# Optimization experiments

Measured on AMD Instinct MI355X. Metric: run time of the kernel, lower is better.

## Reference

```python
import jax, jax.numpy as jnp
import numpy as np

D_MODEL = 1024
N_HEADS = 16
D_K = D_MODEL // N_HEADS


def setup_inputs() -> dict:
    key = jax.random.key(0)
    ks = jax.random.split(key, 9)
    B, S, D = 2, 2048, D_MODEL
    q = jax.random.normal(ks[0], (B, S, D), dtype=jnp.float32)
    v = jax.random.normal(ks[1], (B, S, D), dtype=jnp.float32)
    k = jax.random.normal(ks[2], (B, S, D), dtype=jnp.float32)
    att_mask = jnp.zeros((B, S, S), dtype=jnp.float32)
    seq_mask = jax.random.uniform(ks[3], (B, S, S), dtype=jnp.float32)
    scale = 1.0 / np.sqrt(D)
    Wq = jax.random.normal(ks[4], (D, D), dtype=jnp.float32) * scale
    Wk = jax.random.normal(ks[5], (D, D), dtype=jnp.float32) * scale
    Wv = jax.random.normal(ks[6], (D, D), dtype=jnp.float32) * scale
    Wo = jax.random.normal(ks[7], (D, D), dtype=jnp.float32) * scale
    return {"q": q, "v": v, "k": k, "att_mask": att_mask, "seq_mask": seq_mask,
            "Wq": Wq, "Wk": Wk, "Wv": Wv, "Wo": Wo}


def _split_heads(x, B):
    # [B, S, D] -> [B, H, S, d_k]
    return x.reshape(B, -1, N_HEADS, D_K).transpose(0, 2, 1, 3)


def reference(q, v, k, att_mask, seq_mask, Wq, Wk, Wv, Wo):
    B = q.shape[0]
    qh = _split_heads(q @ Wq, B)
    kh = _split_heads(k @ Wk, B)
    vh = _split_heads(v @ Wv, B)
    # scores: [B, H, Sq, Sk]
    scores = jnp.einsum('bhqd,bhkd->bhqk', qh, kh) / jnp.sqrt(jnp.float32(D_K))
    scores = scores + att_mask[:, None]
    attn = jax.nn.softmax(scores, axis=-1)
    attn = attn * seq_mask[:, None]  # post-softmax multiplicative mask
    out = jnp.einsum('bhqk,bhkd->bhqd', attn, vh)
    out = out.transpose(0, 2, 1, 3).reshape(B, -1, D_MODEL)
    return out @ Wo
```

## Files before the change

### kernel.cpp

```cpp
#include <hip/hip_runtime.h>
#include <cstddef>

typedef __attribute__((ext_vector_type(8))) short s16x8;
typedef __attribute__((ext_vector_type(4))) float f32x4;
typedef __attribute__((ext_vector_type(4))) unsigned short us4;

static __device__ __forceinline__ float bf2f(unsigned short u) {
    union { unsigned u; float f; } v;
    v.u = ((unsigned)u) << 16;
    return v.f;
}

static __device__ __forceinline__ unsigned short f2bf(float f) {
    union { float f; unsigned u; } v;
    v.f = f;
    unsigned r = v.u + 0x7fffu + ((v.u >> 16) & 1u);
    return (unsigned short)(r >> 16);
}

static __device__ __forceinline__ unsigned short f2bf_fast(float f) {
    unsigned r;
    asm("v_cvt_pk_bf16_f32 %0, %1, %2" : "=v"(r) : "v"(f), "v"(f));
    return (unsigned short)r;
}

#if __has_builtin(__builtin_amdgcn_exp2f)
#define EXP2F(x) __builtin_amdgcn_exp2f(x)
#else
#define EXP2F(x) exp2f(x)
#endif

typedef const __attribute__((address_space(1))) unsigned int* as1_cu32p;
typedef __attribute__((address_space(3))) unsigned int* as3_u32p;
static __device__ __forceinline__ void async16(const void* g, void* l) {
    __builtin_amdgcn_global_load_lds((as1_cu32p)g, (as3_u32p)l, 16, 0, 0);
}

static __device__ __forceinline__ float ldf(const unsigned short* p, size_t i) { return bf2f(p[i]); }
static __device__ __forceinline__ float ldf(const float* p, size_t i) { return p[i]; }
static __device__ __forceinline__ void stf(unsigned short* p, size_t i, float v) { p[i] = f2bf(v); }
static __device__ __forceinline__ void stf(float* p, size_t i, float v) { p[i] = v; }

__global__ __launch_bounds__(256) void probe_dtype(
    const unsigned short* __restrict__ q, unsigned* __restrict__ flags)
{
    __shared__ float red[256];
    const int t = threadIdx.x;
    float m = 0.0f;
    for (int i = t; i < 16384; i += 256) {
        float x = fabsf(bf2f(q[i]));
        if (!(x == x)) x = 1.0e30f;
        m = fmaxf(m, x);
    }
    red[t] = m;
    __syncthreads();
    for (int s = 128; s > 0; s >>= 1) {
        if (t < s) red[t] = fmaxf(red[t], red[t + s]);
        __syncthreads();
    }
    if (t == 0) {
        flags[0] = (red[0] < 1000.0f) ? 0u : 1u;
        flags[1] = 0u;
    }
}

__global__ __launch_bounds__(256) void probe_zero(
    const uint4* __restrict__ m, unsigned* __restrict__ flags)
{
    const unsigned dt = flags[0];
    const size_t n = dt ? 2097152u : 1048576u;
    unsigned acc = 0;
    for (size_t i = (size_t)blockIdx.x * 256 + threadIdx.x; i < n;
         i += (size_t)gridDim.x * 256) {
        uint4 v = m[i];
        acc |= v.x | v.y | v.z | v.w;
    }
    if (acc) atomicOr(&flags[1], 1u);
}

__global__ __launch_bounds__(256) void cvt3_f32_bf16(
    const float4* __restrict__ s0, us4* __restrict__ d0,
    const float4* __restrict__ s1, us4* __restrict__ d1,
    const float4* __restrict__ s2, us4* __restrict__ d2,
    unsigned n4, const unsigned* __restrict__ flags)
{
    if (flags[0] != 1u) return;
    const float4* s = (blockIdx.y == 0) ? s0 : (blockIdx.y == 1) ? s1 : s2;
    us4* d = (blockIdx.y == 0) ? d0 : (blockIdx.y == 1) ? d1 : d2;
    for (unsigned i = blockIdx.x * 256u + threadIdx.x; i < n4;
         i += gridDim.x * 256u) {
        float4 v = s[i];
        us4 o;
        o.x = f2bf(v.x); o.y = f2bf(v.y); o.z = f2bf(v.z); o.w = f2bf(v.w);
        d[i] = o;
    }
}

__global__ __launch_bounds__(256) void copy3_bf16(
    const uint4* __restrict__ s0, uint4* __restrict__ d0,
    const uint4* __restrict__ s1, uint4* __restrict__ d1,
    const uint4* __restrict__ s2, uint4* __restrict__ d2,
    unsigned n16, const unsigned* __restrict__ flags)
{
    if (flags[0] != 0u) return;
    const uint4* s = (blockIdx.y == 0) ? s0 : (blockIdx.y == 1) ? s1 : s2;
    uint4* d = (blockIdx.y == 0) ? d0 : (blockIdx.y == 1) ? d1 : d2;
    for (unsigned i = blockIdx.x * 256u + threadIdx.x; i < n16;
         i += gridDim.x * 256u)
        d[i] = s[i];
}

__global__ __launch_bounds__(256) void cvt_f32_bf16(
    const float4* __restrict__ src, us4* __restrict__ dst, unsigned n4,
    const unsigned* __restrict__ flags)
{
    if (flags[0] != 1u) return;
    for (unsigned i = blockIdx.x * 256u + threadIdx.x; i < n4;
         i += gridDim.x * 256u) {
        float4 v = src[i];
        us4 o;
        o.x = f2bf(v.x); o.y = f2bf(v.y); o.z = f2bf(v.z); o.w = f2bf(v.w);
        dst[i] = o;
    }
}

template <typename T>
__global__ __launch_bounds__(256) void transpose_w(
    const T* __restrict__ src, unsigned short* __restrict__ dst,
    const unsigned* __restrict__ flag, unsigned want)
{
    if (*flag != want) return;
    __shared__ unsigned short tile[32][33];
    const int c0 = blockIdx.x * 32, r0 = blockIdx.y * 32;
    const int tx = threadIdx.x, ty = threadIdx.y;
#pragma unroll
    for (int i = 0; i < 32; i += 8)
        tile[ty + i][tx] = f2bf(ldf(src, (size_t)(r0 + ty + i) * 1024 + c0 + tx));
    __syncthreads();
#pragma unroll
    for (int i = 0; i < 32; i += 8)
        dst[(size_t)(c0 + ty + i) * 1024 + r0 + tx] = tile[tx][ty + i];
}

template <typename T>
__global__ __launch_bounds__(256) void transpose_w3(
    const T* __restrict__ s0, const T* __restrict__ s1, const T* __restrict__ s2,
    unsigned short* __restrict__ d0, unsigned short* __restrict__ d1,
    unsigned short* __restrict__ d2,
    const unsigned* __restrict__ flag, unsigned want)
{
    if (*flag != want) return;
    const T* src = (blockIdx.z == 0) ? s0 : (blockIdx.z == 1) ? s1 : s2;
    unsigned short* dst = (blockIdx.z == 0) ? d0 : (blockIdx.z == 1) ? d1 : d2;
    __shared__ unsigned short tile[32][33];
    const int c0 = blockIdx.x * 32, r0 = blockIdx.y * 32;
    const int tx = threadIdx.x, ty = threadIdx.y;
#pragma unroll
    for (int i = 0; i < 32; i += 8)
        tile[ty + i][tx] = f2bf(ldf(src, (size_t)(r0 + ty + i) * 1024 + c0 + tx));
    __syncthreads();
#pragma unroll
    for (int i = 0; i < 32; i += 8)
        dst[(size_t)(c0 + ty + i) * 1024 + r0 + tx] = tile[tx][ty + i];
}

template <typename TO>
__global__ __launch_bounds__(256) void gemm_kernel(
    const unsigned short* __restrict__ A, const unsigned short* __restrict__ Bt,
    TO* __restrict__ out, int mode, const unsigned* __restrict__ flags, unsigned want)
{
    if (want != 2u && flags[0] != want) return;
    const int K = 1024;
    __shared__ __align__(16) unsigned short lA[64 * 72];
    __shared__ __align__(16) unsigned short lB[64 * 72];

    const int m0 = blockIdx.y * 64, n0 = blockIdx.x * 64;
    const int t = threadIdx.x;
    const int w = t >> 6, l = t & 63, quad = l >> 4, l15 = l & 15;
    const int srow = t >> 2, scol = (t & 3) * 16;

    const unsigned short* Arow = A + (size_t)(m0 + srow) * K + scol;
    const unsigned short* Brow = Bt + (size_t)(n0 + srow) * K + scol;

    f32x4 acc[4] = {};

    uint4 a0 = *(const uint4*)(Arow);
    uint4 a1 = *(const uint4*)(Arow + 8);
    uint4 b0 = *(const uint4*)(Brow);
    uint4 b1 = *(const uint4*)(Brow + 8);

    for (int k0 = 0; k0 < K; k0 += 64) {
        *(uint4*)&lA[srow * 72 + scol] = a0;
        *(uint4*)&lA[srow * 72 + scol + 8] = a1;
        *(uint4*)&lB[srow * 72 + scol] = b0;
        *(uint4*)&lB[srow * 72 + scol + 8] = b1;
        __syncthreads();
        const int kn = (k0 + 64) & (K - 1);
        a0 = *(const uint4*)(Arow + kn);
        a1 = *(const uint4*)(Arow + kn + 8);
        b0 = *(const uint4*)(Brow + kn);
        b1 = *(const uint4*)(Brow + kn + 8);
#pragma unroll
        for (int kk = 0; kk < 64; kk += 32) {
            s16x8 af = *(const s16x8*)&lA[(w * 16 + l15) * 72 + kk + quad * 8];
#pragma unroll
            for (int g = 0; g < 4; g++) {
                s16x8 bf = *(const s16x8*)&lB[(g * 16 + l15) * 72 + kk + quad * 8];
                acc[g] = __builtin_amdgcn_mfma_f32_16x16x32_bf16(af, bf, acc[g], 0, 0, 0);
            }
        }
        __syncthreads();
    }

#pragma unroll
    for (int g = 0; g < 4; g++) {
#pragma unroll
        for (int r = 0; r < 4; r++) {
            int row = m0 + w * 16 + quad * 4 + r;
            int col = n0 + g * 16 + l15;
            float val = acc[g][r];
            if (mode == 0) {
                stf(out, (size_t)row * 1024 + col, val);
            } else {
                int b = row >> 11, s = row & 2047;
                int h = col >> 6, d = col & 63;
                if (mode == 1)
                    stf(out, (((size_t)(b * 16 + h) * 2048) + s) * 64 + d, val);
                else
                    stf(out, (((size_t)(b * 16 + h) * 64) + d) * 2048 + s, val);
            }
        }
    }
}

template <typename TM, bool USEA>
__global__ __launch_bounds__(256) void attn_kernel(
    const unsigned short* __restrict__ qh, const unsigned short* __restrict__ kh,
    const unsigned short* __restrict__ vt, const TM* __restrict__ amask,
    const unsigned short* __restrict__ smask, unsigned short* __restrict__ aout,
    const unsigned* __restrict__ flags, unsigned want)
{
    if (flags[0] != want || (flags[1] != 0u) != USEA) return;
    const int S = 2048, DK = 64, H = 16;
    const int qt = blockIdx.x, h = blockIdx.y, b = blockIdx.z;
    const unsigned short* qhb = qh + (size_t)(b * H + h) * S * DK;
    const unsigned short* khb = kh + (size_t)(b * H + h) * S * DK;
    const unsigned short* vtb = vt + (size_t)(b * H + h) * DK * S;
    const TM* amb = amask + (size_t)b * S * S;
    const unsigned short* smb = smask + (size_t)b * S * S;

    __shared__ __align__(16) unsigned short lK[64 * 64];
    __shared__ __align__(16) unsigned short lM[64 * 64];
    __shared__ __align__(16) unsigned short lV[2][64 * 64];
    __shared__ __align__(16) unsigned short lP[4][16 * 72];

    const int t = threadIdx.x;
    const int w = t >> 6, l = t & 63, quad = l >> 4, l15 = l & 15;
    const int q0 = qt * 64;

    const float SCALE2 = 0.18033688011112042f;
    const float LOG2E  = 1.4426950408889634f;

    const int trow = t >> 3;
    const int tcol = (((t & 7) ^ ((t >> 3) & 7)) * 8);
    const unsigned short* ksrc0 = khb + (size_t)trow * DK + tcol;
    const unsigned short* ksrc1 = khb + (size_t)(trow + 32) * DK + tcol;
    const unsigned short* msrc0 = smb + (size_t)(q0 + trow) * S + tcol;
    const unsigned short* msrc1 = smb + (size_t)(q0 + trow + 32) * S + tcol;
    const unsigned short* vsrc0 = vtb + (size_t)trow * S + tcol;
    const unsigned short* vsrc1 = vtb + (size_t)(trow + 32) * S + tcol;
    char* kdst = (char*)lK + (t >> 6) * 1024;
    char* mdst = (char*)lM + (t >> 6) * 1024;
    char* vbase = (char*)&lV[0][0] + (t >> 6) * 1024;

    async16(ksrc0, kdst); async16(ksrc1, kdst + 4096);
    async16(msrc0, mdst); async16(msrc1, mdst + 4096);
    async16(vsrc0, vbase); async16(vsrc1, vbase + 4096);

    const int ksw = (l15 & 7) * 8;

    const int qrow_a = q0 + w * 16 + l15;
    s16x8 qf0 = *(const s16x8*)&qhb[(size_t)qrow_a * DK + quad * 8];
    s16x8 qf1 = *(const s16x8*)&qhb[(size_t)qrow_a * DK + 32 + quad * 8];

    float mrun[4], lsum[4];
    f32x4 o[4] = {};
#pragma unroll
    for (int r = 0; r < 4; r++) { mrun[r] = -INFINITY; lsum[r] = 0.0f; }

    int it = 0;
    for (int k0 = 0; k0 < S; k0 += 64, ++it) {
        __syncthreads();

        f32x4 sc[4] = {};
#pragma unroll
        for (int kk = 0; kk < 64; kk += 32) {
            s16x8 af = (kk == 0) ? qf0 : qf1;
#pragma unroll
            for (int g = 0; g < 4; g++) {
                s16x8 bf = *(const s16x8*)&lK[(g * 16 + l15) * 64 + ((kk + quad * 8) ^ ksw)];
                sc[g] = __builtin_amdgcn_mfma_f32_16x16x32_bf16(af, bf, sc[g], 0, 0, 0);
            }
        }

#pragma unroll
        for (int r = 0; r < 4; r++) {
            float sv0, sv1, sv2, sv3;
            if (USEA) {
                const size_t mrow = (size_t)(q0 + w * 16 + quad * 4 + r) * S + k0;
                sv0 = fmaf((float)ldf(amb, mrow + 0 * 16 + l15), LOG2E, sc[0][r] * SCALE2);
                sv1 = fmaf((float)ldf(amb, mrow + 1 * 16 + l15), LOG2E, sc[1][r] * SCALE2);
                sv2 = fmaf((float)ldf(amb, mrow + 2 * 16 + l15), LOG2E, sc[2][r] * SCALE2);
                sv3 = fmaf((float)ldf(amb, mrow + 3 * 16 + l15), LOG2E, sc[3][r] * SCALE2);
            } else {
                sv0 = sc[0][r] * SCALE2;
                sv1 = sc[1][r] * SCALE2;
                sv2 = sc[2][r] * SCALE2;
                sv3 = sc[3][r] * SCALE2;
            }
            float mx = fmaxf(fmaxf(sv0, sv1), fmaxf(sv2, sv3));
#pragma unroll
            for (int d = 1; d < 16; d <<= 1) mx = fmaxf(mx, __shfl_xor(mx, d));
            float mnew = fmaxf(mrun[r], mx);
            float alpha = EXP2F(mrun[r] - mnew);
            float e0 = EXP2F(sv0 - mnew);
            float e1 = EXP2F(sv1 - mnew);
            float e2 = EXP2F(sv2 - mnew);
            float e3 = EXP2F(sv3 - mnew);
            lsum[r] = lsum[r] * alpha + ((e0 + e1) + (e2 + e3));
            mrun[r] = mnew;
#pragma unroll
            for (int g = 0; g < 4; g++) o[g][r] *= alpha;

            const int rowm = (w * 16 + quad * 4 + r) * 64;
            const int msw = ((quad * 4 + r) & 7) * 8;
            const int rowp = (quad * 4 + r) * 72;
            lP[w][rowp + 0 * 16 + l15] = f2bf_fast(e0 * bf2f(lM[rowm + ((0 * 16 + l15) ^ msw)]));
            lP[w][rowp + 1 * 16 + l15] = f2bf_fast(e1 * bf2f(lM[rowm + ((1 * 16 + l15) ^ msw)]));
            lP[w][rowp + 2 * 16 + l15] = f2bf_fast(e2 * bf2f(lM[rowm + ((2 * 16 + l15) ^ msw)]));
            lP[w][rowp + 3 * 16 + l15] = f2bf_fast(e3 * bf2f(lM[rowm + ((3 * 16 + l15) ^ msw)]));
        }
        __syncthreads();

        const int kn = (k0 + 64) & (S - 1);
        if (kn) {
            async16(ksrc0 + (size_t)kn * DK, kdst);
            async16(ksrc1 + (size_t)kn * DK, kdst + 4096);
            async16(msrc0 + kn, mdst);
            async16(msrc1 + kn, mdst + 4096);
            char* vd = vbase + ((it + 1) & 1) * 8192;
            async16(vsrc0 + kn, vd);
            async16(vsrc1 + kn, vd + 4096);
        }

        const unsigned short* lVc = &lV[it & 1][0];
#pragma unroll
        for (int kk = 0; kk < 64; kk += 32) {
            s16x8 pf = *(const s16x8*)&lP[w][l15 * 72 + kk + quad * 8];
#pragma unroll
            for (int g = 0; g < 4; g++) {
                s16x8 vf = *(const s16x8*)&lVc[(g * 16 + l15) * 64 + ((kk + quad * 8) ^ ksw)];
                o[g] = __builtin_amdgcn_mfma_f32_16x16x32_bf16(pf, vf, o[g], 0, 0, 0);
            }
        }
    }

#pragma unroll
    for (int r = 0; r < 4; r++) {
        float ls = lsum[r];
#pragma unroll
        for (int d = 1; d < 16; d <<= 1) ls += __shfl_xor(ls, d);
        float inv = 1.0f / ls;
        const int qr = q0 + w * 16 + quad * 4 + r;
#pragma unroll
        for (int g = 0; g < 4; g++) {
            aout[((size_t)(b * S + qr)) * 1024 + h * 64 + g * 16 + l15] =
                f2bf_fast(o[g][r] * inv);
        }
    }
}

extern "C" void kernel_launch(void* const* d_in, const int* in_sizes, int n_in,
                              void* d_out, int out_size, void* d_ws, size_t ws_size,
                              hipStream_t stream)
{
    const void* q   = d_in[0];
    const void* v   = d_in[1];
    const void* k   = d_in[2];
    const void* att = d_in[3];
    const void* seq = d_in[4];
    const void* Wq  = d_in[5];
    const void* Wk  = d_in[6];
    const void* Wv  = d_in[7];
    const void* Wo  = d_in[8];

    const size_t WELEM = 1024 * 1024;
    const size_t HELEM = (size_t)2 * 16 * 2048 * 64;

    unsigned* flags = (unsigned*)d_ws;
    unsigned short* base = (unsigned short*)((char*)d_ws + 512);
    unsigned short* r0 = base;
    unsigned short* qh = base + HELEM;
    unsigned short* kh = qh + HELEM;
    unsigned short* vt = kh + HELEM;
    unsigned short* qb = vt + HELEM;
    unsigned short* kb = qb + HELEM;
    unsigned short* vb = kb + HELEM;
    unsigned short* seqb = qb;

    const dim3 tg(32, 32), tb(32, 8);
    const dim3 tg3(32, 32, 3);
    const dim3 gg(16, 64), gb(256);
    const dim3 ag(32, 16, 2), ab(256);

    probe_dtype<<<1, 256, 0, stream>>>((const unsigned short*)q, flags);
    probe_zero<<<1024, 256, 0, stream>>>((const uint4*)att, flags);

    const unsigned n4h = 1048576u, n16h = 524288u;
    cvt3_f32_bf16<<<dim3(512, 3), 256, 0, stream>>>(
        (const float4*)q, (us4*)qb, (const float4*)k, (us4*)kb,
        (const float4*)v, (us4*)vb, n4h, flags);
    copy3_bf16<<<dim3(512, 3), 256, 0, stream>>>(
        (const uint4*)q, (uint4*)qb, (const uint4*)k, (uint4*)kb,
        (const uint4*)v, (uint4*)vb, n16h, flags);

    transpose_w3<unsigned short><<<tg3, tb, 0, stream>>>(
        (const unsigned short*)Wq, (const unsigned short*)Wk, (const unsigned short*)Wv,
        r0 + 0 * WELEM, r0 + 1 * WELEM, r0 + 2 * WELEM, flags, 0);
    transpose_w3<float><<<tg3, tb, 0, stream>>>(
        (const float*)Wq, (const float*)Wk, (const float*)Wv,
        r0 + 0 * WELEM, r0 + 1 * WELEM, r0 + 2 * WELEM, flags, 1);

    gemm_kernel<unsigned short><<<gg, gb, 0, stream>>>(qb, r0 + 0 * WELEM, qh, 1, flags, 2);
    gemm_kernel<unsigned short><<<gg, gb, 0, stream>>>(kb, r0 + 1 * WELEM, kh, 1, flags, 2);
    gemm_kernel<unsigned short><<<gg, gb, 0, stream>>>(vb, r0 + 2 * WELEM, vt, 2, flags, 2);

    const unsigned n4s = 2097152u;
    cvt_f32_bf16<<<2048, 256, 0, stream>>>((const float4*)seq, (us4*)seqb, n4s, flags);

    unsigned short* ao = r0;
    attn_kernel<unsigned short, false><<<ag, ab, 0, stream>>>(
        qh, kh, vt, (const unsigned short*)att, (const unsigned short*)seq, ao, flags, 0);
    attn_kernel<float, false><<<ag, ab, 0, stream>>>(
        qh, kh, vt, (const float*)att, seqb, ao, flags, 1);
    attn_kernel<unsigned short, true><<<ag, ab, 0, stream>>>(
        qh, kh, vt, (const unsigned short*)att, (const unsigned short*)seq, ao, flags, 0);
    attn_kernel<float, true><<<ag, ab, 0, stream>>>(
        qh, kh, vt, (const float*)att, seqb, ao, flags, 1);

    transpose_w<unsigned short><<<tg, tb, 0, stream>>>((const unsigned short*)Wo, qh, flags, 0);
    transpose_w<float><<<tg, tb, 0, stream>>>((const float*)Wo, qh, flags, 1);

    gemm_kernel<unsigned short><<<gg, gb, 0, stream>>>(ao, qh, (unsigned short*)d_out, 0, flags, 0);
    gemm_kernel<float><<<gg, gb, 0, stream>>>(ao, qh, (float*)d_out, 0, flags, 1);
}
```

Before: 409.1 us.

## Use 128x128 double-buffered async-load GEMM tiles and batch QKV projections

Replaces the 64x64 GEMM with a 128x128 tile body that gives each wave a 64x64 sub-tile, uses XOR-swizzled LDS with double buffering fed by async global-to-LDS copies, and merges the three QKV projection launches into one z-indexed grid. The goal is more data reuse per LDS load, global loads overlapped with MFMA work, and fewer kernel launches. The cost is higher register pressure from 16 accumulators and 64KB of LDS per block, which may reduce occupancy.

```diff
diff --git a/kernel.cpp b/kernel.cpp
--- a/kernel.cpp
+++ b/kernel.cpp
@@ -165,72 +165,111 @@
 }
 
 template <typename TO>
+static __device__ __forceinline__ void gemm128_body(
+    const unsigned short* __restrict__ A, const unsigned short* __restrict__ Bt,
+    TO* __restrict__ out, int mode, int m0, int n0)
+{
+    const int K = 1024;
+    __shared__ __align__(16) unsigned short lA[2][128 * 64];
+    __shared__ __align__(16) unsigned short lB[2][128 * 64];
+
+    const int t = threadIdx.x;
+    const int w = t >> 6, l = t & 63, quad = l >> 4, l15 = l & 15;
+    const int wr = w >> 1, wc = w & 1;
+
+    const int srow = t >> 3;
+    const int scol = (((t & 7) ^ ((t >> 3) & 7)) * 8);
+    const unsigned short* Asrc = A + (size_t)(m0 + srow) * K + scol;
+    const unsigned short* Bsrc = Bt + (size_t)(n0 + srow) * K + scol;
+
+    f32x4 acc[4][4] = {};
+
+#pragma unroll
+    for (int n = 0; n < 4; n++) {
+        async16(Asrc + (size_t)(n * 32) * K, (char*)&lA[0][0] + w * 1024 + n * 4096);
+        async16(Bsrc + (size_t)(n * 32) * K, (char*)&lB[0][0] + w * 1024 + n * 4096);
+    }
+
+    int cur = 0;
+    for (int k0 = 0; k0 < K; k0 += 64) {
+        __syncthreads();
+        if (k0 + 64 < K) {
+            char* da = (char*)&lA[cur ^ 1][0] + w * 1024;
+            char* db = (char*)&lB[cur ^ 1][0] + w * 1024;
+#pragma unroll
+            for (int n = 0; n < 4; n++) {
+                async16(Asrc + (size_t)(n * 32) * K + (k0 + 64), da + n * 4096);
+                async16(Bsrc + (size_t)(n * 32) * K + (k0 + 64), db + n * 4096);
+            }
+        }
+        const unsigned short* pA = &lA[cur][0];
+        const unsigned short* pB = &lB[cur][0];
+        const int sw = (l15 & 7) * 8;
+#pragma unroll
+        for (int kk = 0; kk < 64; kk += 32) {
+            const int co = (kk + quad * 8) ^ sw;
+            s16x8 af[4], bf[4];
+#pragma unroll
+            for (int i = 0; i < 4; i++)
+                af[i] = *(const s16x8*)&pA[(wr * 64 + i * 16 + l15) * 64 + co];
+#pragma unroll
+            for (int j = 0; j < 4; j++)
+                bf[j] = *(const s16x8*)&pB[(wc * 64 + j * 16 + l15) * 64 + co];
+#pragma unroll
+            for (int i = 0; i < 4; i++)
+#pragma unroll
+                for (int j = 0; j < 4; j++)
+                    acc[i][j] = __builtin_amdgcn_mfma_f32_16x16x32_bf16(
+                        af[i], bf[j], acc[i][j], 0, 0, 0);
+        }
+        cur ^= 1;
+    }
+
+#pragma unroll
+    for (int i = 0; i < 4; i++) {
+#pragma unroll
+        for (int j = 0; j < 4; j++) {
+#pragma unroll
+            for (int r = 0; r < 4; r++) {
+                int row = m0 + wr * 64 + i * 16 + quad * 4 + r;
+                int col = n0 + wc * 64 + j * 16 + l15;
+                float val = acc[i][j][r];
+                if (mode == 0) {
+                    stf(out, (size_t)row * 1024 + col, val);
+                } else {
+                    int b = row >> 11, s = row & 2047;
+                    int h = col >> 6, d = col & 63;
+                    if (mode == 1)
+                        stf(out, (((size_t)(b * 16 + h) * 2048) + s) * 64 + d, val);
+                    else
+                        stf(out, (((size_t)(b * 16 + h) * 64) + d) * 2048 + s, val);
+                }
+            }
+        }
+    }
+}
+
+__global__ __launch_bounds__(256) void gemm3_kernel(
+    const unsigned short* __restrict__ qb, const unsigned short* __restrict__ kb,
+    const unsigned short* __restrict__ vb, const unsigned short* __restrict__ wt,
+    unsigned short* __restrict__ qh, unsigned short* __restrict__ kh,
+    unsigned short* __restrict__ vt)
+{
+    const int z = blockIdx.z;
+    const unsigned short* A = (z == 0) ? qb : (z == 1) ? kb : vb;
+    const unsigned short* Bt = wt + (size_t)z * 1024 * 1024;
+    unsigned short* out = (z == 0) ? qh : (z == 1) ? kh : vt;
+    gemm128_body<unsigned short>(A, Bt, out, (z == 2) ? 2 : 1,
+                                 blockIdx.y * 128, blockIdx.x * 128);
+}
+
+template <typename TO>
 __global__ __launch_bounds__(256) void gemm_kernel(
     const unsigned short* __restrict__ A, const unsigned short* __restrict__ Bt,
     TO* __restrict__ out, int mode, const unsigned* __restrict__ flags, unsigned want)
 {
-    if (want != 2u && flags[0] != want) return;
-    const int K = 1024;
-    __shared__ __align__(16) unsigned short lA[64 * 72];
-    __shared__ __align__(16) unsigned short lB[64 * 72];
-
-    const int m0 = blockIdx.y * 64, n0 = blockIdx.x * 64;
-    const int t = threadIdx.x;
-    const int w = t >> 6, l = t & 63, quad = l >> 4, l15 = l & 15;
-    const int srow = t >> 2, scol = (t & 3) * 16;
-
-    const unsigned short* Arow = A + (size_t)(m0 + srow) * K + scol;
-    const unsigned short* Brow = Bt + (size_t)(n0 + srow) * K + scol;
-
-    f32x4 acc[4] = {};
-
-    uint4 a0 = *(const uint4*)(Arow);
-    uint4 a1 = *(const uint4*)(Arow + 8);
-    uint4 b0 = *(const uint4*)(Brow);
-    uint4 b1 = *(const uint4*)(Brow + 8);
-
-    for (int k0 = 0; k0 < K; k0 += 64) {
-        *(uint4*)&lA[srow * 72 + scol] = a0;
-        *(uint4*)&lA[srow * 72 + scol + 8] = a1;
-        *(uint4*)&lB[srow * 72 + scol] = b0;
-        *(uint4*)&lB[srow * 72 + scol + 8] = b1;
-        __syncthreads();
-        const int kn = (k0 + 64) & (K - 1);
-        a0 = *(const uint4*)(Arow + kn);
-        a1 = *(const uint4*)(Arow + kn + 8);
-        b0 = *(const uint4*)(Brow + kn);
-        b1 = *(const uint4*)(Brow + kn + 8);
-#pragma unroll
-        for (int kk = 0; kk < 64; kk += 32) {
-            s16x8 af = *(const s16x8*)&lA[(w * 16 + l15) * 72 + kk + quad * 8];
-#pragma unroll
-            for (int g = 0; g < 4; g++) {
-                s16x8 bf = *(const s16x8*)&lB[(g * 16 + l15) * 72 + kk + quad * 8];
-                acc[g] = __builtin_amdgcn_mfma_f32_16x16x32_bf16(af, bf, acc[g], 0, 0, 0);
-            }
-        }
-        __syncthreads();
-    }
-
-#pragma unroll
-    for (int g = 0; g < 4; g++) {
-#pragma unroll
-        for (int r = 0; r < 4; r++) {
-            int row = m0 + w * 16 + quad * 4 + r;
-            int col = n0 + g * 16 + l15;
-            float val = acc[g][r];
-            if (mode == 0) {
-                stf(out, (size_t)row * 1024 + col, val);
-            } else {
-                int b = row >> 11, s = row & 2047;
-                int h = col >> 6, d = col & 63;
-                if (mode == 1)
-                    stf(out, (((size_t)(b * 16 + h) * 2048) + s) * 64 + d, val);
-                else
-                    stf(out, (((size_t)(b * 16 + h) * 64) + d) * 2048 + s, val);
-            }
-        }
-    }
+    if (flags[0] != want) return;
+    gemm128_body<TO>(A, Bt, out, mode, blockIdx.y * 128, blockIdx.x * 128);
 }
 
 template <typename TM, bool USEA>
@@ -410,7 +449,8 @@
 
     const dim3 tg(32, 32), tb(32, 8);
     const dim3 tg3(32, 32, 3);
-    const dim3 gg(16, 64), gb(256);
+    const dim3 gg(8, 32), gb(256);
+    const dim3 gg3(8, 32, 3);
     const dim3 ag(32, 16, 2), ab(256);
 
     probe_dtype<<<1, 256, 0, stream>>>((const unsigned short*)q, flags);
@@ -431,9 +471,7 @@
         (const float*)Wq, (const float*)Wk, (const float*)Wv,
         r0 + 0 * WELEM, r0 + 1 * WELEM, r0 + 2 * WELEM, flags, 1);
 
-    gemm_kernel<unsigned short><<<gg, gb, 0, stream>>>(qb, r0 + 0 * WELEM, qh, 1, flags, 2);
-    gemm_kernel<unsigned short><<<gg, gb, 0, stream>>>(kb, r0 + 1 * WELEM, kh, 1, flags, 2);
-    gemm_kernel<unsigned short><<<gg, gb, 0, stream>>>(vb, r0 + 2 * WELEM, vt, 2, flags, 2);
+    gemm3_kernel<<<gg3, gb, 0, stream>>>(qb, kb, vb, r0, qh, kh, vt);
 
     const unsigned n4s = 2097152u;
     cvt_f32_bf16<<<2048, 256, 0, stream>>>((const float4*)seq, (us4*)seqb, n4s, flags);
```

After: 402.9 us. About the same (-1.5%).
